# Kernel optimization log

Measured on AMD Instinct MI355X. Metric: run time of the kernel, lower is better.

The kernel has to match this reference:

```python
import jax, jax.numpy as jnp
import numpy as np

TEMPERATURE = 0.1
LISTWISE_W = 1.0
HARD_NEG_K = 32
MARGIN = 0.5
PAIRWISE_W = 0.5
NEG = jnp.float32(-1e30)  # finite stand-in for -inf (avoids inf-inf NaNs)


def _masked_segment_lse(vals, mask, idx, num_segments):
    """Stable segment-wise logsumexp over vals where mask is True."""
    v = jnp.where(mask, vals, NEG)
    m = jax.ops.segment_max(v, idx, num_segments=num_segments)  # [G]
    ex = jnp.where(mask, jnp.exp(vals - m[idx]), 0.0)
    s = jax.ops.segment_sum(ex, idx, num_segments=num_segments)
    tiny = jnp.finfo(vals.dtype).tiny
    return m + jnp.log(jnp.maximum(s, tiny))


def setup_inputs() -> dict:
    key = jax.random.key(0)
    k1, k2 = jax.random.split(key)
    G, L = 4096, 512  # graphs x edges-per-graph
    E = G * L
    logits = jax.random.normal(k1, (E,), dtype=jnp.float32)
    targets = (jax.random.uniform(k2, (E,)) < 0.1).astype(jnp.float32)
    edge_batch = jnp.repeat(jnp.arange(G, dtype=jnp.int32), L)  # sorted segment ids
    return {"logits": logits, "targets": targets, "edge_batch": edge_batch, "num_graphs": G}


def reference(logits, targets, edge_batch, num_graphs):
    G = int(num_graphs)
    E = logits.shape[0]
    L = E // G  # equal-size segments by construction

    # ---- listwise term ----
    scaled = logits / TEMPERATURE
    all_mask = jnp.ones_like(logits, dtype=bool)
    log_denom = _masked_segment_lse(scaled, all_mask, edge_batch, G)
    # (every graph has edges here, so the has_edge zeroing in torch is a no-op)
    pos_mask = targets > 0.5
    log_num = _masked_segment_lse(scaled, pos_mask, edge_batch, G)
    pos_cnt = jax.ops.segment_sum(pos_mask.astype(jnp.float32), edge_batch, num_segments=G)
    has_pos = pos_cnt > 0
    log_num_safe = jnp.where(has_pos, log_num, log_denom)
    listwise_den = jnp.maximum(jnp.sum(has_pos.astype(jnp.float32)), 1.0)
    listwise = jnp.sum(-(log_num_safe - log_denom)) / listwise_den

    # ---- pairwise hard-negative term ----
    k = HARD_NEG_K
    lg = logits.reshape(G, L)
    pos2 = (targets > 0.5).reshape(G, L)
    neg_vals = jnp.where(pos2, NEG, lg)
    hard, _ = jax.lax.top_k(neg_vals, k)  # [G, k], descending
    neg_cnt = jnp.sum(~pos2, axis=1)
    kg = jnp.minimum(neg_cnt, k)  # per-graph k = min(hard_neg_k, #neg)
    valid_n = jnp.arange(k)[None, :] < kg[:, None]  # [G, k]
    hard = jnp.where(valid_n, hard, NEG)
    # softplus(margin + z_n - z_p) over pos p x top-k negatives n: [G, L, k]
    pair = jax.nn.softplus(MARGIN + hard[:, None, :] - lg[:, :, None])
    pm = pos2[:, :, None] & valid_n[:, None, :]
    psum = jnp.sum(jnp.where(pm, pair, 0.0), axis=(1, 2))  # [G]
    Pg = jnp.sum(pos2, axis=1).astype(jnp.float32)
    kgf = kg.astype(jnp.float32)
    active = (Pg > 0) & (kgf > 0)
    contrib = jnp.where(active, psum / jnp.maximum(Pg * kgf, 1.0), 0.0)
    n_pg = jnp.sum(active.astype(jnp.float32))
    pairwise = jnp.sum(contrib) / jnp.maximum(n_pg, 1.0)

    return LISTWISE_W * listwise + PAIRWISE_W * pairwise
```

## Files before the change

kernel.cpp:

```cpp
#include <hip/hip_runtime.h>
#include <math.h>

#define L        512
#define BLK      64
#define KTOP     32
#define NEGV     (-1e30f)

#define LOG2E    1.4426950408889634f
#define LOG2E10  14.426950408889634f
#define LN2      0.6931471805599453f
#define M_L2E    0.7213475204444817f

#if __has_builtin(__builtin_amdgcn_exp2f)
#define EXP2F(x) __builtin_amdgcn_exp2f(x)
#else
#define EXP2F(x) exp2f(x)
#endif
#if __has_builtin(__builtin_amdgcn_logf)
#define LOG2F(x) __builtin_amdgcn_logf(x)
#else
#define LOG2F(x) __log2f(x)
#endif

__device__ __forceinline__ float softplus_l2(float x2) {
    return fmaxf(x2, 0.0f) + LOG2F(1.0f + EXP2F(fminf(x2, -x2)));
}

__device__ __forceinline__ unsigned lanes_below(unsigned long long m) {
    return __builtin_amdgcn_mbcnt_hi((unsigned)(m >> 32),
           __builtin_amdgcn_mbcnt_lo((unsigned)(m & 0xffffffffull), 0u));
}

__global__ __launch_bounds__(BLK) void graph_loss_kernel(
    const float* __restrict__ logits,
    const float* __restrict__ targets,
    float4* __restrict__ partials )
{
    __shared__ float pos_s[L];
    __shared__ float hard_s[KTOP];

    const int lane = threadIdx.x;
    const int g    = blockIdx.x;

    const float4* lg4 = (const float4*)(logits  + (size_t)g * L);
    const float4* tg4 = (const float4*)(targets + (size_t)g * L);
    const float4 la = lg4[lane * 2], lb = lg4[lane * 2 + 1];
    const float4 ta = tg4[lane * 2], tb = tg4[lane * 2 + 1];
    float v[8]  = {la.x, la.y, la.z, la.w, lb.x, lb.y, lb.z, lb.w};
    float tv[8] = {ta.x, ta.y, ta.z, ta.w, tb.x, tb.y, tb.z, tb.w};
    bool  p[8];
    unsigned nu[8];

#pragma unroll
    for (int e = 0; e < 8; e++) {
        p[e] = tv[e] > 0.5f;
        const unsigned i = __float_as_uint(v[e]);
        const unsigned msk = (unsigned)((int)i >> 31) | 0x80000000u;
        nu[e] = p[e] ? 0u : (i ^ msk);
    }

    int pbase = 0;
#pragma unroll
    for (int e = 0; e < 8; e++) {
        const unsigned long long m = __ballot((int)p[e]);
        if (p[e]) pos_s[pbase + lanes_below(m)] = v[e] * LOG2E;
        pbase += __popcll(m);
    }
    const int P = pbase;

    float u[8];
    float s_mx = NEGV;
#pragma unroll
    for (int e = 0; e < 8; e++) {
        u[e] = v[e] * LOG2E10;
        s_mx = fmaxf(s_mx, u[e]);
    }
#pragma unroll
    for (int off = 32; off; off >>= 1)
        s_mx = fmaxf(s_mx, __shfl_xor(s_mx, off, 64));

    float se_all = 0.0f, se_pos = 0.0f;
#pragma unroll
    for (int e = 0; e < 8; e++) {
        const float ep = EXP2F(u[e] - s_mx);
        se_all += ep;
        se_pos += p[e] ? ep : 0.0f;
    }
#pragma unroll
    for (int off = 32; off; off >>= 1) {
        se_all += __shfl_xor(se_all, off, 64);
        se_pos += __shfl_xor(se_pos, off, 64);
    }

    float lw = 0.0f, contrib = 0.0f, hp = 0.0f, act = 0.0f;
    if (P > 0) {
        hp = 1.0f;
        lw = LN2 * (LOG2F(se_all) - LOG2F(se_pos));
    }
    const int neg_cnt = L - P;
    const int K = neg_cnt < KTOP ? neg_cnt : KTOP;

    if (P > 0 && K > 0) {
        unsigned prefix = 0u;
        int exact = 0;
        for (int b = 31; b >= 0; --b) {
            const unsigned cand = prefix | (1u << b);
            int cnt = 0;
#pragma unroll
            for (int e = 0; e < 8; e++)
                cnt += __popcll(__ballot(nu[e] >= cand));
            if (cnt >= K) {
                prefix = cand;
                if (cnt == K) { exact = 1; break; }
            }
        }
        const unsigned lo = prefix - (unsigned)exact;
        const unsigned ti = prefix ^ ((prefix & 0x80000000u) ? 0x80000000u
                                                             : 0xFFFFFFFFu);
        const float tval = __uint_as_float(ti);
        const float tc2  = fmaf(tval, LOG2E, M_L2E);

        int hbase = 0;
#pragma unroll
        for (int e = 0; e < 8; e++) {
            const bool gt = nu[e] > lo;
            const unsigned long long m = __ballot((int)gt);
            if (gt) hard_s[hbase + lanes_below(m)] = fmaf(v[e], LOG2E, M_L2E);
            hbase += __popcll(m);
        }
        const int c_gt = hbase;

        float psum = 0.0f;
        if (K == KTOP) {
            const float hc = (lane < c_gt) ? hard_s[lane & (KTOP - 1)] : tc2;
            for (int base = 0; base < P; base += 64) {
                const float qs = pos_s[base + lane];
                float a0 = 0.0f, a1 = 0.0f, a2 = 0.0f, a3 = 0.0f;
#pragma unroll
                for (int n = 0; n < KTOP; n += 4) {
                    a0 += softplus_l2(__shfl(hc, n + 0, 64) - qs);
                    a1 += softplus_l2(__shfl(hc, n + 1, 64) - qs);
                    a2 += softplus_l2(__shfl(hc, n + 2, 64) - qs);
                    a3 += softplus_l2(__shfl(hc, n + 3, 64) - qs);
                }
                const float s = (a0 + a1) + (a2 + a3);
                psum += (base + lane < P) ? s : 0.0f;
            }
        } else {
            for (int n = 0; n < c_gt; n++) {
                const float c2 = hard_s[n];
                for (int pp = lane; pp < P; pp += 64)
                    psum += softplus_l2(c2 - pos_s[pp]);
            }
            if (K > c_gt) {
                float t = 0.0f;
                for (int pp = lane; pp < P; pp += 64)
                    t += softplus_l2(tc2 - pos_s[pp]);
                psum += (float)(K - c_gt) * t;
            }
        }
#pragma unroll
        for (int off = 32; off; off >>= 1)
            psum += __shfl_xor(psum, off, 64);
        contrib = LN2 * psum / fmaxf((float)P * (float)K, 1.0f);
        act = 1.0f;
    }

    if (lane == 0) partials[g] = make_float4(lw, hp, contrib, act);
}

__global__ __launch_bounds__(256) void finalize_kernel(
    const float4* __restrict__ partials, int n, float* __restrict__ out)
{
    float s0 = 0, s1 = 0, s2 = 0, s3 = 0;
    for (int i = threadIdx.x; i < n; i += 256) {
        const float4 p = partials[i];
        s0 += p.x; s1 += p.y; s2 += p.z; s3 += p.w;
    }
#pragma unroll
    for (int off = 32; off; off >>= 1) {
        s0 += __shfl_xor(s0, off, 64);
        s1 += __shfl_xor(s1, off, 64);
        s2 += __shfl_xor(s2, off, 64);
        s3 += __shfl_xor(s3, off, 64);
    }
    __shared__ float red[4][4];
    const int lane = threadIdx.x & 63, wid = threadIdx.x >> 6;
    if (lane == 0) { red[wid][0]=s0; red[wid][1]=s1; red[wid][2]=s2; red[wid][3]=s3; }
    __syncthreads();
    if (threadIdx.x == 0) {
        const float a0 = red[0][0]+red[1][0]+red[2][0]+red[3][0];
        const float a1 = red[0][1]+red[1][1]+red[2][1]+red[3][1];
        const float a2 = red[0][2]+red[1][2]+red[2][2]+red[3][2];
        const float a3 = red[0][3]+red[1][3]+red[2][3]+red[3][3];
        const float listwise = a0 / fmaxf(a1, 1.0f);
        const float pairwise = a2 / fmaxf(a3, 1.0f);
        out[0] = 1.0f * listwise + 0.5f * pairwise;
    }
}

extern "C" void kernel_launch(void* const* d_in, const int* in_sizes, int n_in,
                              void* d_out, int out_size, void* d_ws, size_t ws_size,
                              hipStream_t stream) {
    const float* logits  = (const float*)d_in[0];
    const float* targets = (const float*)d_in[1];
    const int E = in_sizes[0];
    const int G = E / L;

    float4* partials = (float4*)d_ws;
    graph_loss_kernel<<<G, BLK, 0, stream>>>(logits, targets, partials);
    finalize_kernel<<<1, 256, 0, stream>>>(partials, G, (float*)d_out);
}
```

Before: 88.22 us.

## Pack four graphs per 256-thread block with in-block partial reduction

Each block now runs four wavefronts, one graph per wavefront, instead of one 64-thread block per graph. Per-wave results are combined in shared memory so only one partial float4 is written per block, which cuts the finalize kernel's input by a factor of four. The aim is lower block launch and scheduling overhead and a cheaper final reduction. In exchange, a block-wide barrier means the fastest waves wait for the slowest graph in their block, and the block needs more shared memory.

```diff
diff --git a/kernel.cpp b/kernel.cpp
--- a/kernel.cpp
+++ b/kernel.cpp
@@ -2,7 +2,8 @@
 #include <math.h>
 
 #define L        512
-#define BLK      64
+#define BLK      256
+#define WPB      4
 #define KTOP     32
 #define NEGV     (-1e30f)
 
@@ -34,147 +35,167 @@
 __global__ __launch_bounds__(BLK) void graph_loss_kernel(
     const float* __restrict__ logits,
     const float* __restrict__ targets,
-    float4* __restrict__ partials )
+    int G,
+    float* __restrict__ partials )
 {
-    __shared__ float pos_s[L];
-    __shared__ float hard_s[KTOP];
-
-    const int lane = threadIdx.x;
-    const int g    = blockIdx.x;
-
-    const float4* lg4 = (const float4*)(logits  + (size_t)g * L);
-    const float4* tg4 = (const float4*)(targets + (size_t)g * L);
-    const float4 la = lg4[lane * 2], lb = lg4[lane * 2 + 1];
-    const float4 ta = tg4[lane * 2], tb = tg4[lane * 2 + 1];
-    float v[8]  = {la.x, la.y, la.z, la.w, lb.x, lb.y, lb.z, lb.w};
-    float tv[8] = {ta.x, ta.y, ta.z, ta.w, tb.x, tb.y, tb.z, tb.w};
-    bool  p[8];
-    unsigned nu[8];
-
-#pragma unroll
-    for (int e = 0; e < 8; e++) {
-        p[e] = tv[e] > 0.5f;
-        const unsigned i = __float_as_uint(v[e]);
-        const unsigned msk = (unsigned)((int)i >> 31) | 0x80000000u;
-        nu[e] = p[e] ? 0u : (i ^ msk);
-    }
-
-    int pbase = 0;
-#pragma unroll
-    for (int e = 0; e < 8; e++) {
-        const unsigned long long m = __ballot((int)p[e]);
-        if (p[e]) pos_s[pbase + lanes_below(m)] = v[e] * LOG2E;
-        pbase += __popcll(m);
-    }
-    const int P = pbase;
-
-    float u[8];
-    float s_mx = NEGV;
-#pragma unroll
-    for (int e = 0; e < 8; e++) {
-        u[e] = v[e] * LOG2E10;
-        s_mx = fmaxf(s_mx, u[e]);
-    }
-#pragma unroll
-    for (int off = 32; off; off >>= 1)
-        s_mx = fmaxf(s_mx, __shfl_xor(s_mx, off, 64));
-
-    float se_all = 0.0f, se_pos = 0.0f;
-#pragma unroll
-    for (int e = 0; e < 8; e++) {
-        const float ep = EXP2F(u[e] - s_mx);
-        se_all += ep;
-        se_pos += p[e] ? ep : 0.0f;
-    }
-#pragma unroll
-    for (int off = 32; off; off >>= 1) {
-        se_all += __shfl_xor(se_all, off, 64);
-        se_pos += __shfl_xor(se_pos, off, 64);
-    }
+    __shared__ float pos_s[WPB][L];
+    __shared__ float hard_s[WPB][KTOP];
+    __shared__ float wres[WPB][4];
+
+    const int tid  = threadIdx.x;
+    const int lane = tid & 63;
+    const int w    = tid >> 6;
+    const int g    = blockIdx.x * WPB + w;
+    const bool valid = (g < G);
 
     float lw = 0.0f, contrib = 0.0f, hp = 0.0f, act = 0.0f;
-    if (P > 0) {
-        hp = 1.0f;
-        lw = LN2 * (LOG2F(se_all) - LOG2F(se_pos));
-    }
-    const int neg_cnt = L - P;
-    const int K = neg_cnt < KTOP ? neg_cnt : KTOP;
-
-    if (P > 0 && K > 0) {
-        unsigned prefix = 0u;
-        int exact = 0;
-        for (int b = 31; b >= 0; --b) {
-            const unsigned cand = prefix | (1u << b);
-            int cnt = 0;
-#pragma unroll
-            for (int e = 0; e < 8; e++)
-                cnt += __popcll(__ballot(nu[e] >= cand));
-            if (cnt >= K) {
-                prefix = cand;
-                if (cnt == K) { exact = 1; break; }
+
+    if (valid) {
+        const float4* lg4 = (const float4*)(logits  + (size_t)g * L);
+        const float4* tg4 = (const float4*)(targets + (size_t)g * L);
+        const float4 la = lg4[lane * 2], lb = lg4[lane * 2 + 1];
+        const float4 ta = tg4[lane * 2], tb = tg4[lane * 2 + 1];
+        float v[8]  = {la.x, la.y, la.z, la.w, lb.x, lb.y, lb.z, lb.w};
+        float tv[8] = {ta.x, ta.y, ta.z, ta.w, tb.x, tb.y, tb.z, tb.w};
+        bool  p[8];
+        unsigned nu[8];
+
+#pragma unroll
+        for (int e = 0; e < 8; e++) {
+            p[e] = tv[e] > 0.5f;
+            const unsigned i = __float_as_uint(v[e]);
+            const unsigned msk = (unsigned)((int)i >> 31) | 0x80000000u;
+            nu[e] = p[e] ? 0u : (i ^ msk);
+        }
+
+        int pbase = 0;
+#pragma unroll
+        for (int e = 0; e < 8; e++) {
+            const unsigned long long m = __ballot((int)p[e]);
+            if (p[e]) pos_s[w][pbase + lanes_below(m)] = v[e] * LOG2E;
+            pbase += __popcll(m);
+        }
+        const int P = pbase;
+
+        float u[8];
+        float s_mx = NEGV;
+#pragma unroll
+        for (int e = 0; e < 8; e++) {
+            u[e] = v[e] * LOG2E10;
+            s_mx = fmaxf(s_mx, u[e]);
+        }
+#pragma unroll
+        for (int off = 32; off; off >>= 1)
+            s_mx = fmaxf(s_mx, __shfl_xor(s_mx, off, 64));
+
+        float se_all = 0.0f, se_pos = 0.0f;
+#pragma unroll
+        for (int e = 0; e < 8; e++) {
+            const float ep = EXP2F(u[e] - s_mx);
+            se_all += ep;
+            se_pos += p[e] ? ep : 0.0f;
+        }
+#pragma unroll
+        for (int off = 32; off; off >>= 1) {
+            se_all += __shfl_xor(se_all, off, 64);
+            se_pos += __shfl_xor(se_pos, off, 64);
+        }
+
+        if (P > 0) {
+            hp = 1.0f;
+            lw = LN2 * (LOG2F(se_all) - LOG2F(se_pos));
+        }
+        const int neg_cnt = L - P;
+        const int K = neg_cnt < KTOP ? neg_cnt : KTOP;
+
+        if (P > 0 && K > 0) {
+            unsigned prefix = 0u;
+            int exact = 0;
+            for (int b = 31; b >= 0; --b) {
+                const unsigned cand = prefix | (1u << b);
+                int cnt = 0;
+#pragma unroll
+                for (int e = 0; e < 8; e++)
+                    cnt += __popcll(__ballot(nu[e] >= cand));
+                if (cnt >= K) {
+                    prefix = cand;
+                    if (cnt == K) { exact = 1; break; }
+                }
             }
-        }
-        const unsigned lo = prefix - (unsigned)exact;
-        const unsigned ti = prefix ^ ((prefix & 0x80000000u) ? 0x80000000u
-                                                             : 0xFFFFFFFFu);
-        const float tval = __uint_as_float(ti);
-        const float tc2  = fmaf(tval, LOG2E, M_L2E);
-
-        int hbase = 0;
-#pragma unroll
-        for (int e = 0; e < 8; e++) {
-            const bool gt = nu[e] > lo;
-            const unsigned long long m = __ballot((int)gt);
-            if (gt) hard_s[hbase + lanes_below(m)] = fmaf(v[e], LOG2E, M_L2E);
-            hbase += __popcll(m);
-        }
-        const int c_gt = hbase;
-
-        float psum = 0.0f;
-        if (K == KTOP) {
-            const float hc = (lane < c_gt) ? hard_s[lane & (KTOP - 1)] : tc2;
-            for (int base = 0; base < P; base += 64) {
-                const float qs = pos_s[base + lane];
-                float a0 = 0.0f, a1 = 0.0f, a2 = 0.0f, a3 = 0.0f;
-#pragma unroll
-                for (int n = 0; n < KTOP; n += 4) {
-                    a0 += softplus_l2(__shfl(hc, n + 0, 64) - qs);
-                    a1 += softplus_l2(__shfl(hc, n + 1, 64) - qs);
-                    a2 += softplus_l2(__shfl(hc, n + 2, 64) - qs);
-                    a3 += softplus_l2(__shfl(hc, n + 3, 64) - qs);
-                }
-                const float s = (a0 + a1) + (a2 + a3);
-                psum += (base + lane < P) ? s : 0.0f;
+            const unsigned lo = prefix - (unsigned)exact;
+            const unsigned ti = prefix ^ ((prefix & 0x80000000u) ? 0x80000000u
+                                                                 : 0xFFFFFFFFu);
+            const float tval = __uint_as_float(ti);
+            const float tc2  = fmaf(tval, LOG2E, M_L2E);
+
+            int hbase = 0;
+#pragma unroll
+            for (int e = 0; e < 8; e++) {
+                const bool gt = nu[e] > lo;
+                const unsigned long long m = __ballot((int)gt);
+                if (gt) hard_s[w][hbase + lanes_below(m)] =
+                            fmaf(v[e], LOG2E, M_L2E);
+                hbase += __popcll(m);
             }
-        } else {
-            for (int n = 0; n < c_gt; n++) {
-                const float c2 = hard_s[n];
-                for (int pp = lane; pp < P; pp += 64)
-                    psum += softplus_l2(c2 - pos_s[pp]);
+            const int c_gt = hbase;
+
+            float psum = 0.0f;
+            if (K == KTOP) {
+                const float hc = (lane < c_gt) ? hard_s[w][lane & (KTOP - 1)]
+                                               : tc2;
+                for (int base = 0; base < P; base += 64) {
+                    const float qs = pos_s[w][base + lane];
+                    float a0 = 0.0f, a1 = 0.0f, a2 = 0.0f, a3 = 0.0f;
+#pragma unroll
+                    for (int n = 0; n < KTOP; n += 4) {
+                        a0 += softplus_l2(__shfl(hc, n + 0, 64) - qs);
+                        a1 += softplus_l2(__shfl(hc, n + 1, 64) - qs);
+                        a2 += softplus_l2(__shfl(hc, n + 2, 64) - qs);
+                        a3 += softplus_l2(__shfl(hc, n + 3, 64) - qs);
+                    }
+                    const float s = (a0 + a1) + (a2 + a3);
+                    psum += (base + lane < P) ? s : 0.0f;
+                }
+            } else {
+                for (int n = 0; n < c_gt; n++) {
+                    const float c2 = hard_s[w][n];
+                    for (int pp = lane; pp < P; pp += 64)
+                        psum += softplus_l2(c2 - pos_s[w][pp]);
+                }
+                if (K > c_gt) {
+                    float t = 0.0f;
+                    for (int pp = lane; pp < P; pp += 64)
+                        t += softplus_l2(tc2 - pos_s[w][pp]);
+                    psum += (float)(K - c_gt) * t;
+                }
             }
-            if (K > c_gt) {
-                float t = 0.0f;
-                for (int pp = lane; pp < P; pp += 64)
-                    t += softplus_l2(tc2 - pos_s[pp]);
-                psum += (float)(K - c_gt) * t;
-            }
-        }
-#pragma unroll
-        for (int off = 32; off; off >>= 1)
-            psum += __shfl_xor(psum, off, 64);
-        contrib = LN2 * psum / fmaxf((float)P * (float)K, 1.0f);
-        act = 1.0f;
-    }
-
-    if (lane == 0) partials[g] = make_float4(lw, hp, contrib, act);
+#pragma unroll
+            for (int off = 32; off; off >>= 1)
+                psum += __shfl_xor(psum, off, 64);
+            contrib = LN2 * psum / fmaxf((float)P * (float)K, 1.0f);
+            act = 1.0f;
+        }
+    }
+
+    if (lane == 0) {
+        wres[w][0] = lw;
+        wres[w][1] = hp;
+        wres[w][2] = contrib;
+        wres[w][3] = act;
+    }
+    __syncthreads();
+    if (tid < 4) {
+        partials[blockIdx.x * 4 + tid] =
+            wres[0][tid] + wres[1][tid] + wres[2][tid] + wres[3][tid];
+    }
 }
 
 __global__ __launch_bounds__(256) void finalize_kernel(
-    const float4* __restrict__ partials, int n, float* __restrict__ out)
+    const float* __restrict__ partials, int nblocks, float* __restrict__ out)
 {
     float s0 = 0, s1 = 0, s2 = 0, s3 = 0;
-    for (int i = threadIdx.x; i < n; i += 256) {
-        const float4 p = partials[i];
+    for (int i = threadIdx.x; i < nblocks; i += 256) {
+        const float4 p = ((const float4*)partials)[i];
         s0 += p.x; s1 += p.y; s2 += p.z; s3 += p.w;
     }
 #pragma unroll
@@ -206,8 +227,9 @@
     const float* targets = (const float*)d_in[1];
     const int E = in_sizes[0];
     const int G = E / L;
-
-    float4* partials = (float4*)d_ws;
-    graph_loss_kernel<<<G, BLK, 0, stream>>>(logits, targets, partials);
-    finalize_kernel<<<1, 256, 0, stream>>>(partials, G, (float*)d_out);
-}
+    const int nblocks = (G + WPB - 1) / WPB;
+
+    float* partials = (float*)d_ws;
+    graph_loss_kernel<<<nblocks, BLK, 0, stream>>>(logits, targets, G, partials);
+    finalize_kernel<<<1, 256, 0, stream>>>(partials, nblocks, (float*)d_out);
+}
```

After: 81.18 us (median of 2 runs). -8.0%, faster.
